# Kernel tuning notes

Hardware: AMD Instinct MI355X
Metric: run time of the kernel (lower is better)

Reference implementation:

```python
import jax, jax.numpy as jnp
import numpy as np

N, L, H, D = 8, 1024, 16, 64
HD = H * D          # hidden_size = 1024
MLP = 4 * HD        # mlp_dim = 4096
EPS = 1e-5


def _layer_norm(x, g, b):
    mu = jnp.mean(x, axis=-1, keepdims=True)
    var = jnp.var(x, axis=-1, keepdims=True)
    return (x - mu) * jax.lax.rsqrt(var + EPS) * g + b


def setup_inputs() -> dict:
    key = jax.random.key(0)
    ks = jax.random.split(key, 8)
    s_in = 1.0 / np.sqrt(HD)
    s_mlp = 1.0 / np.sqrt(MLP)
    return {
        "x": jax.random.normal(ks[0], (N, L, HD), jnp.float32),
        "ln0_g": jnp.ones((HD,), jnp.float32),
        "ln0_b": jnp.zeros((HD,), jnp.float32),
        "wq": jax.random.normal(ks[1], (HD, HD), jnp.float32) * s_in,
        "bq": jnp.zeros((HD,), jnp.float32),
        "wk": jax.random.normal(ks[2], (HD, HD), jnp.float32) * s_in,
        "bk": jnp.zeros((HD,), jnp.float32),
        "wv": jax.random.normal(ks[3], (HD, HD), jnp.float32) * s_in,
        "bv": jnp.zeros((HD,), jnp.float32),
        "wo": jax.random.normal(ks[4], (HD, HD), jnp.float32) * s_in,
        "bo": jnp.zeros((HD,), jnp.float32),
        "ln1_g": jnp.ones((HD,), jnp.float32),
        "ln1_b": jnp.zeros((HD,), jnp.float32),
        "w1": jax.random.normal(ks[5], (HD, MLP), jnp.float32) * s_in,
        "b1": jnp.zeros((MLP,), jnp.float32),
        "w2": jax.random.normal(ks[6], (MLP, HD), jnp.float32) * s_mlp,
        "b2": jnp.zeros((HD,), jnp.float32),
    }


def reference(x, ln0_g, ln0_b, wq, bq, wk, bk, wv, bv, wo, bo,
              ln1_g, ln1_b, w1, b1, w2, b2):
    n, l, hd = x.shape
    # --- pre-LN self-attention ---
    y = _layer_norm(x, ln0_g, ln0_b)
    q = (y @ wq + bq).reshape(n, l, H, D)
    k = (y @ wk + bk).reshape(n, l, H, D)
    v = (y @ wv + bv).reshape(n, l, H, D)
    qkt = jnp.einsum('nqhd,nkhd->nqkh', q, k) / jnp.sqrt(jnp.float32(D))
    attn = jax.nn.softmax(qkt, axis=2)
    y = jnp.einsum('nqkh,nkhd->nqhd', attn, v).reshape(n, l, hd)
    y = y @ wo + bo
    x = x + y  # residual (dropout_rate=0 in eval)
    # --- pre-LN MLP ---
    y = _layer_norm(x, ln1_g, ln1_b)
    y = jax.nn.gelu(y @ w1 + b1)
    y = y @ w2 + b2
    return x + y
```

## Files before the change

kernel.cpp:

```cpp
#include <hip/hip_runtime.h>
#include <math.h>

typedef __attribute__((ext_vector_type(8))) __bf16 bf16x8;
typedef __attribute__((ext_vector_type(4))) float f32x4;

#define NBATCH 8
#define SEQ    1024
#define NHEAD  16
#define DHEAD  64
#define HID    1024
#define MLPD   4096

static __device__ __forceinline__ unsigned short f2bf(float f) {
  unsigned int u = __float_as_uint(f);
  u += 0x7fffu + ((u >> 16) & 1u);
  return (unsigned short)(u >> 16);
}

static __device__ __forceinline__ void gload_lds16(const unsigned short* g,
                                                   unsigned short* l) {
  __builtin_amdgcn_global_load_lds(
      (const __attribute__((address_space(1))) unsigned int*)g,
      (__attribute__((address_space(3))) unsigned int*)l, 16, 0, 0);
}

static __device__ __forceinline__ float gelu_fast(float v) {
  const float z = 0.7978845608028654f * (v + 0.044715f * v * v * v);
  const float e = __expf(-2.0f * fabsf(z));
  float th = (1.0f - e) / (1.0f + e);
  th = copysignf(th, z);
  return 0.5f * v * (1.0f + th);
}

#define MFMA16(a, b, c) __builtin_amdgcn_mfma_f32_16x16x32_bf16(a, b, c, 0, 0, 0)

__global__ __launch_bounds__(256) void k_transpose(const float* __restrict__ in,
                                                   unsigned short* __restrict__ out,
                                                   int R, int C) {
  __shared__ float t[32][33];
  const int tx = threadIdx.x & 31, ty = threadIdx.x >> 5;
  const int c0 = blockIdx.x * 32, r0 = blockIdx.y * 32;
#pragma unroll
  for (int j = 0; j < 4; ++j)
    t[ty + j * 8][tx] = in[(size_t)(r0 + ty + j * 8) * C + c0 + tx];
  __syncthreads();
#pragma unroll
  for (int j = 0; j < 4; ++j)
    out[(size_t)(c0 + ty + j * 8) * R + r0 + tx] = f2bf(t[tx][ty + j * 8]);
}

__global__ void k_pack_bias(const float* __restrict__ bq, const float* __restrict__ bk,
                            const float* __restrict__ bv, float* __restrict__ o) {
  int i = blockIdx.x * 256 + threadIdx.x;
  if (i < 3 * HID) {
    float v = (i < HID) ? bq[i] : (i < 2 * HID ? bk[i - HID] : bv[i - 2 * HID]);
    o[i] = v;
  }
}

__global__ __launch_bounds__(256) void k_ln(const float* __restrict__ x,
                                            const float* __restrict__ gw,
                                            const float* __restrict__ bw,
                                            unsigned short* __restrict__ y) {
  __shared__ float red[2][4];
  const int row = blockIdx.x;
  const int tid = threadIdx.x;
  const float4 v = ((const float4*)(x + (size_t)row * HID))[tid];
  float sum = v.x + v.y + v.z + v.w;
  float sq  = v.x * v.x + v.y * v.y + v.z * v.z + v.w * v.w;
#pragma unroll
  for (int off = 32; off >= 1; off >>= 1) {
    sum += __shfl_xor(sum, off);
    sq  += __shfl_xor(sq, off);
  }
  if ((tid & 63) == 0) { red[0][tid >> 6] = sum; red[1][tid >> 6] = sq; }
  __syncthreads();
  sum = red[0][0] + red[0][1] + red[0][2] + red[0][3];
  sq  = red[1][0] + red[1][1] + red[1][2] + red[1][3];
  const float mu  = sum * (1.0f / HID);
  const float var = sq * (1.0f / HID) - mu * mu;
  const float rs  = rsqrtf(var + 1e-5f);
  const float4 g4 = ((const float4*)gw)[tid];
  const float4 b4 = ((const float4*)bw)[tid];
  ushort4 ov;
  ov.x = f2bf((v.x - mu) * rs * g4.x + b4.x);
  ov.y = f2bf((v.y - mu) * rs * g4.y + b4.y);
  ov.z = f2bf((v.z - mu) * rs * g4.z + b4.z);
  ov.w = f2bf((v.w - mu) * rs * g4.w + b4.w);
  ((ushort4*)(y + (size_t)row * HID))[tid] = ov;
}

template <int EPI, int BN>
__global__ __launch_bounds__(512, 2) void k_gemm(const unsigned short* __restrict__ A,
                                                 const unsigned short* __restrict__ BT,
                                                 const float* __restrict__ bias,
                                                 const float* __restrict__ res,
                                                 void* __restrict__ Cout,
                                                 int M, int N, int K) {
  constexpr int ASZ = 256 * 64;
  constexpr int BSZ = BN * 64;
  constexpr int NF  = BN / 64;
  constexpr int NCW = BN / 4;
  __shared__ unsigned short sh[2 * ASZ + 2 * BSZ];

  const int tid  = threadIdx.x;
  const int lane = tid & 63;
  const int w    = tid >> 6;
  const int wr   = w >> 2, wc = w & 3;
  const int l15  = lane & 15, g = lane >> 4;

  const int gx = gridDim.x;
  const int nwg = gx * gridDim.y;
  int lid = blockIdx.y * gx + blockIdx.x;
  lid = (lid & 7) * (nwg >> 3) + (lid >> 3);
  const int m0 = (lid / gx) * 256, n0 = (lid % gx) * BN;

  f32x4 acc[8][NF] = {};

  const int srow  = w * 8 + (lane >> 3);
  const int scolb = ((lane & 7) * 16) ^ (((lane >> 3) & 7) << 4);
  const unsigned short* pA = A  + (size_t)(m0 + srow) * K + (scolb >> 1);
  const unsigned short* pB = BT + (size_t)(n0 + srow) * K + (scolb >> 1);
  unsigned short* shB = sh + 2 * ASZ;

#define STAGE(buf_, kk)                                                     \
  do {                                                                      \
    _Pragma("unroll") for (int c = 0; c < 4; ++c)                           \
      gload_lds16(pA + (size_t)c * 64 * K + (kk),                           \
                  sh + (buf_) * ASZ + (c * 64 + w * 8) * 64);               \
    _Pragma("unroll") for (int c = 0; c < BN / 64; ++c)                     \
      gload_lds16(pB + (size_t)c * 64 * K + (kk),                           \
                  shB + (buf_) * BSZ + (c * 64 + w * 8) * 64);              \
  } while (0)

  const int fmask = (l15 & 7) << 4;
  const int bo0 = ((0 * 64) + g * 16) ^ fmask;
  const int bo1 = ((1 * 64) + g * 16) ^ fmask;
  const int aRowBase = wr * 128 + l15;
  const int bRowBase = wc * NCW + l15;

  const int NT = K >> 6;

  STAGE(0, 0);
  int buf = 0;
  for (int t = 0; t < NT; ++t) {
    const unsigned short* shAb = sh + buf * ASZ;
    const unsigned short* shBb = shB + buf * BSZ;

    asm volatile("s_waitcnt vmcnt(0)" ::: "memory");
    __builtin_amdgcn_sched_barrier(0);
    __builtin_amdgcn_s_barrier();
    if (t + 1 < NT) STAGE(buf ^ 1, (t + 1) * 64);

    bf16x8 bfr[NF][2];
#pragma unroll
    for (int n = 0; n < NF; ++n) {
      const int br = (bRowBase + n * 16) * 64;
      bfr[n][0] = *(const bf16x8*)(shBb + br + (bo0 >> 1));
      bfr[n][1] = *(const bf16x8*)(shBb + br + (bo1 >> 1));
    }
    bf16x8 afr[8][2];
#pragma unroll
    for (int m = 0; m < 8; ++m) {
      const int ar = (aRowBase + m * 16) * 64;
      afr[m][0] = *(const bf16x8*)(shAb + ar + (bo0 >> 1));
      afr[m][1] = *(const bf16x8*)(shAb + ar + (bo1 >> 1));
    }
    __builtin_amdgcn_sched_barrier(0);

#pragma unroll
    for (int p = 0; p < 4; ++p) {
      __builtin_amdgcn_s_setprio(1);
#pragma unroll
      for (int n = 0; n < NF; ++n) {
        acc[2 * p][n]     = MFMA16(afr[2 * p][0],     bfr[n][0], acc[2 * p][n]);
        acc[2 * p][n]     = MFMA16(afr[2 * p][1],     bfr[n][1], acc[2 * p][n]);
        acc[2 * p + 1][n] = MFMA16(afr[2 * p + 1][0], bfr[n][0], acc[2 * p + 1][n]);
        acc[2 * p + 1][n] = MFMA16(afr[2 * p + 1][1], bfr[n][1], acc[2 * p + 1][n]);
      }
      __builtin_amdgcn_s_setprio(0);
    }
    buf ^= 1;
  }
#undef STAGE

  if constexpr (EPI == 2) {
#pragma unroll
    for (int m = 0; m < 8; ++m) {
#pragma unroll
      for (int n = 0; n < NF; ++n) {
        const int col = n0 + wc * NCW + n * 16 + l15;
        const float bc = bias[col];
#pragma unroll
        for (int r = 0; r < 4; ++r) {
          const int row = m0 + wr * 128 + m * 16 + g * 4 + r;
          const size_t idx = (size_t)row * N + col;
          ((float*)Cout)[idx] = acc[m][n][r] + bc + res[idx];
        }
      }
    }
  } else {
    __builtin_amdgcn_s_barrier();
    unsigned short* ep = sh + w * (128 * NCW);
#pragma unroll
    for (int m = 0; m < 8; ++m) {
#pragma unroll
      for (int n = 0; n < NF; ++n) {
        const float bc = bias[n0 + wc * NCW + n * 16 + l15];
#pragma unroll
        for (int r = 0; r < 4; ++r) {
          float v = acc[m][n][r] + bc;
          if constexpr (EPI == 1) v = gelu_fast(v);
          ep[(m * 16 + g * 4 + r) * NCW + n * 16 + l15] = f2bf(v);
        }
      }
    }
    constexpr int CPR = NCW / 8;
#pragma unroll
    for (int j = 0; j < NCW / 4; ++j) {
      const int t = lane + j * 64;
      const int row = t / CPR, colb = (t % CPR) * 8;
      const uint4 vv = *(const uint4*)(ep + row * NCW + colb);
      unsigned short* outp = (unsigned short*)Cout +
          (size_t)(m0 + wr * 128 + row) * N + n0 + wc * NCW + colb;
      *(uint4*)outp = vv;
    }
  }
}

__global__ __launch_bounds__(256) void k_vt(const unsigned short* __restrict__ qkv,
                                            unsigned short* __restrict__ vT) {
  __shared__ unsigned short t[64][72];
  const int nh = blockIdx.y;
  const int nb = nh >> 4, h = nh & 15;
  const int l0 = blockIdx.x * 64;
  const int tx = threadIdx.x & 7;
  const int ty = threadIdx.x >> 3;
  const unsigned short* src = qkv + (size_t)(nb * SEQ + l0) * 3072 + 2048 + h * DHEAD;
#pragma unroll
  for (int j = 0; j < 2; ++j)
    *(uint4*)(&t[ty + j * 32][tx * 8]) =
        *(const uint4*)(&src[(size_t)(ty + j * 32) * 3072 + tx * 8]);
  __syncthreads();
  unsigned short* dst = vT + (size_t)nh * DHEAD * SEQ + l0;
#pragma unroll
  for (int j = 0; j < 2; ++j) {
    const int d = ty + j * 32;
    ushort4 a, b;
    a.x = t[tx * 8 + 0][d]; a.y = t[tx * 8 + 1][d];
    a.z = t[tx * 8 + 2][d]; a.w = t[tx * 8 + 3][d];
    b.x = t[tx * 8 + 4][d]; b.y = t[tx * 8 + 5][d];
    b.z = t[tx * 8 + 6][d]; b.w = t[tx * 8 + 7][d];
    *(ushort4*)(&dst[(size_t)d * SEQ + tx * 8])     = a;
    *(ushort4*)(&dst[(size_t)d * SEQ + tx * 8 + 4]) = b;
  }
}

#define SOFTMAX_GROUP(S, gq)                                                       \
  {                                                                                \
    float mx = -INFINITY;                                                          \
    _Pragma("unroll") for (int c = 0; c < 4; ++c)                                  \
      _Pragma("unroll") for (int r = 0; r < 4; ++r)                                \
        mx = fmaxf(mx, S[c][r]);                                                   \
    mx = fmaxf(mx, __shfl_xor(mx, 16));                                            \
    mx = fmaxf(mx, __shfl_xor(mx, 32));                                            \
    const float mnew = fmaxf(m_run[gq], mx);                                       \
    const float sc = __expf(0.125f * (m_run[gq] - mnew));                          \
    m_run[gq] = mnew;                                                              \
    float ts = 0.0f;                                                               \
    _Pragma("unroll") for (int c = 0; c < 4; ++c) {                                \
      const float p0 = __expf(0.125f * (S[c][0] - mnew));                          \
      const float p1 = __expf(0.125f * (S[c][1] - mnew));                          \
      const float p2 = __expf(0.125f * (S[c][2] - mnew));                          \
      const float p3 = __expf(0.125f * (S[c][3] - mnew));                          \
      ts += (p0 + p1) + (p2 + p3);                                                 \
      const unsigned int lo = (unsigned int)f2bf(p0) | ((unsigned int)f2bf(p1) << 16); \
      const unsigned int hi = (unsigned int)f2bf(p2) | ((unsigned int)f2bf(p3) << 16); \
      *(uint2*)(&P_lds[w][((gq) * 16 + l15) * 72 + c * 16 + g * 4]) = make_uint2(lo, hi); \
    }                                                                              \
    ts += __shfl_xor(ts, 16);                                                      \
    ts += __shfl_xor(ts, 32);                                                      \
    s_run[gq] = s_run[gq] * sc + ts;                                               \
    const float scr0 = __shfl(sc, g * 4 + 0), scr1 = __shfl(sc, g * 4 + 1);        \
    const float scr2 = __shfl(sc, g * 4 + 2), scr3 = __shfl(sc, g * 4 + 3);        \
    _Pragma("unroll") for (int dt = 0; dt < 4; ++dt) {                             \
      o[gq][dt][0] *= scr0; o[gq][dt][1] *= scr1;                                  \
      o[gq][dt][2] *= scr2; o[gq][dt][3] *= scr3;                                  \
    }                                                                              \
  }

__global__ __launch_bounds__(256, 4) void k_attn(const unsigned short* __restrict__ qkv,
                                                 const unsigned short* __restrict__ vT,
                                                 unsigned short* __restrict__ outp) {
  __shared__ unsigned short Ks[64 * 64];
  __shared__ unsigned short Vs[64 * 64];
  __shared__ unsigned short P_lds[4][32 * 72];
  const int tid  = threadIdx.x;
  const int lane = tid & 63;
  const int w    = tid >> 6;
  const int l15  = lane & 15, g = lane >> 4;
  const int nh = blockIdx.y;
  const int nb = nh >> 4, h = nh & 15;
  const int q0 = blockIdx.x * 128 + w * 32;
  const size_t RS = 3 * HID;

  const unsigned short* Qp = qkv + (size_t)(nb * SEQ + q0) * RS + h * DHEAD;
  const unsigned short* Kg = qkv + (size_t)(nb * SEQ) * RS + HID + h * DHEAD;
  const unsigned short* Vg = vT + (size_t)nh * DHEAD * SEQ;

  const int L0 = tid * 32, L1 = L0 + 16;
  const int kr0 = L0 >> 7, kc0 = (L0 & 127) ^ ((kr0 & 7) << 4);
  const int kr1 = L1 >> 7, kc1 = (L1 & 127) ^ ((kr1 & 7) << 4);

  bf16x8 aq[2][2];
#pragma unroll
  for (int gq = 0; gq < 2; ++gq)
#pragma unroll
    for (int t = 0; t < 2; ++t)
      aq[gq][t] = *(const bf16x8*)(&Qp[(size_t)(gq * 16 + l15) * RS + t * 32 + g * 8]);

  f32x4 o[2][4] = {};
  float m_run[2] = {-INFINITY, -INFINITY};
  float s_run[2] = {0.0f, 0.0f};

  uint4 rk0, rk1, rv0, rv1;
  rk0 = *(const uint4*)(Kg + (size_t)kr0 * RS + (kc0 >> 1));
  rk1 = *(const uint4*)(Kg + (size_t)kr1 * RS + (kc1 >> 1));
  rv0 = *(const uint4*)(Vg + (size_t)kr0 * SEQ + (kc0 >> 1));
  rv1 = *(const uint4*)(Vg + (size_t)kr1 * SEQ + (kc1 >> 1));
  *(uint4*)(&Ks[tid * 16])     = rk0;
  *(uint4*)(&Ks[tid * 16 + 8]) = rk1;
  *(uint4*)(&Vs[tid * 16])     = rv0;
  *(uint4*)(&Vs[tid * 16 + 8]) = rv1;
  __syncthreads();

  const int sw = (l15 & 7) << 4;

  for (int t16 = 0; t16 < 16; ++t16) {
    if (t16 < 15) {
      const int kb = (t16 + 1) * 64;
      rk0 = *(const uint4*)(Kg + (size_t)(kb + kr0) * RS + (kc0 >> 1));
      rk1 = *(const uint4*)(Kg + (size_t)(kb + kr1) * RS + (kc1 >> 1));
      rv0 = *(const uint4*)(Vg + (size_t)kr0 * SEQ + kb + (kc0 >> 1));
      rv1 = *(const uint4*)(Vg + (size_t)kr1 * SEQ + kb + (kc1 >> 1));
    }

    f32x4 S0[4], S1[4];
#pragma unroll
    for (int c = 0; c < 4; ++c) {
      const int krow = c * 16 + l15;
      const bf16x8 k0 = *(const bf16x8*)(&Ks[krow * 64 + ((( 0 + g * 16) ^ sw) >> 1)]);
      const bf16x8 k1 = *(const bf16x8*)(&Ks[krow * 64 + (((64 + g * 16) ^ sw) >> 1)]);
      f32x4 a = {};
      a = MFMA16(k0, aq[0][0], a);
      a = MFMA16(k1, aq[0][1], a);
      S0[c] = a;
      f32x4 b = {};
      b = MFMA16(k0, aq[1][0], b);
      b = MFMA16(k1, aq[1][1], b);
      S1[c] = b;
    }

    SOFTMAX_GROUP(S0, 0)
    SOFTMAX_GROUP(S1, 1)

    bf16x8 pa[2][2];
#pragma unroll
    for (int gq = 0; gq < 2; ++gq)
#pragma unroll
      for (int th = 0; th < 2; ++th)
        pa[gq][th] = *(const bf16x8*)(&P_lds[w][(gq * 16 + l15) * 72 + th * 32 + g * 8]);
#pragma unroll
    for (int dt = 0; dt < 4; ++dt) {
      const int vrow = dt * 16 + l15;
      const bf16x8 v0 = *(const bf16x8*)(&Vs[vrow * 64 + ((( 0 + g * 16) ^ sw) >> 1)]);
      const bf16x8 v1 = *(const bf16x8*)(&Vs[vrow * 64 + (((64 + g * 16) ^ sw) >> 1)]);
      o[0][dt] = MFMA16(pa[0][0], v0, o[0][dt]);
      o[0][dt] = MFMA16(pa[0][1], v1, o[0][dt]);
      o[1][dt] = MFMA16(pa[1][0], v0, o[1][dt]);
      o[1][dt] = MFMA16(pa[1][1], v1, o[1][dt]);
    }
    __syncthreads();
    if (t16 < 15) {
      *(uint4*)(&Ks[tid * 16])     = rk0;
      *(uint4*)(&Ks[tid * 16 + 8]) = rk1;
      *(uint4*)(&Vs[tid * 16])     = rv0;
      *(uint4*)(&Vs[tid * 16 + 8]) = rv1;
      __syncthreads();
    }
  }

#pragma unroll
  for (int gq = 0; gq < 2; ++gq) {
    float sr[4];
#pragma unroll
    for (int r = 0; r < 4; ++r) sr[r] = 1.0f / __shfl(s_run[gq], g * 4 + r);
#pragma unroll
    for (int dt = 0; dt < 4; ++dt)
#pragma unroll
      for (int r = 0; r < 4; ++r)
        outp[(size_t)(nb * SEQ + q0 + gq * 16 + g * 4 + r) * HID + h * DHEAD + dt * 16 + l15] =
            f2bf(o[gq][dt][r] * sr[r]);
  }
}

extern "C" void kernel_launch(void* const* d_in, const int* in_sizes, int n_in,
                              void* d_out, int out_size, void* d_ws, size_t ws_size,
                              hipStream_t stream) {
  const float* x    = (const float*)d_in[0];
  const float* ln0g = (const float*)d_in[1];
  const float* ln0b = (const float*)d_in[2];
  const float* wq   = (const float*)d_in[3];
  const float* bq   = (const float*)d_in[4];
  const float* wk   = (const float*)d_in[5];
  const float* bk   = (const float*)d_in[6];
  const float* wv   = (const float*)d_in[7];
  const float* bv   = (const float*)d_in[8];
  const float* wo   = (const float*)d_in[9];
  const float* bo   = (const float*)d_in[10];
  const float* ln1g = (const float*)d_in[11];
  const float* ln1b = (const float*)d_in[12];
  const float* w1   = (const float*)d_in[13];
  const float* b1   = (const float*)d_in[14];
  const float* w2   = (const float*)d_in[15];
  const float* b2   = (const float*)d_in[16];
  float* out = (float*)d_out;

  char* ws = (char*)d_ws;
  unsigned short* qkvT = (unsigned short*)(ws + 0);
  unsigned short* woT  = (unsigned short*)(ws + 6291456);
  unsigned short* w1T  = (unsigned short*)(ws + 8388608);
  unsigned short* w2T  = (unsigned short*)(ws + 16777216);
  float*          bqkv = (float*)(ws + 25165824);
  unsigned short* ybuf = (unsigned short*)(ws + 25178112);
  unsigned short* qkv  = (unsigned short*)(ws + 41955328);
  unsigned short* att  = (unsigned short*)(ws + 92286976);
  unsigned short* hbuf = qkv;
  unsigned short* vT   = ybuf;

  const int M = NBATCH * SEQ;

  k_transpose<<<dim3(32, 32),  256, 0, stream>>>(wq, qkvT,                        HID,  HID);
  k_transpose<<<dim3(32, 32),  256, 0, stream>>>(wk, qkvT + (size_t)1024 * HID,   HID,  HID);
  k_transpose<<<dim3(32, 32),  256, 0, stream>>>(wv, qkvT + (size_t)2048 * HID,   HID,  HID);
  k_transpose<<<dim3(32, 32),  256, 0, stream>>>(wo, woT,                         HID,  HID);
  k_transpose<<<dim3(128, 32), 256, 0, stream>>>(w1, w1T,                         HID,  MLPD);
  k_transpose<<<dim3(32, 128), 256, 0, stream>>>(w2, w2T,                         MLPD, HID);
  k_pack_bias<<<dim3(12), 256, 0, stream>>>(bq, bk, bv, bqkv);

  k_ln<<<dim3(M), 256, 0, stream>>>(x, ln0g, ln0b, ybuf);
  k_gemm<0, 128><<<dim3(24, 32), 512, 0, stream>>>(ybuf, qkvT, bqkv, nullptr, (void*)qkv, M, 3 * HID, HID);
  k_vt<<<dim3(16, 128), 256, 0, stream>>>(qkv, vT);
  k_attn<<<dim3(8, 128), 256, 0, stream>>>(qkv, vT, att);
  k_gemm<2, 128><<<dim3(8, 32), 512, 0, stream>>>(att, woT, bo, x, (void*)out, M, HID, HID);
  k_ln<<<dim3(M), 256, 0, stream>>>(out, ln1g, ln1b, ybuf);
  k_gemm<1, 256><<<dim3(16, 32), 512, 0, stream>>>(ybuf, w1T, b1, nullptr, (void*)hbuf, M, MLPD, HID);
  k_gemm<2, 128><<<dim3(8, 32), 512, 0, stream>>>(hbuf, w2T, b2, out, (void*)out, M, HID, MLPD);
}
```

Before: 376.8 us.

## Triple-buffer GEMM LDS staging and fix BN at 128 for all GEMMs

Moves the GEMM mainloop from double to triple buffering. Tiles are prefetched two steps ahead, and a partial vmcnt wait lets one stage's loads stay in flight while the current tile is computed. BN is fixed at 128, so the MLP-up GEMM now uses 128-wide tiles with twice as many workgroups. LDS use per block grows to 3*(32KB+16KB)=144KB, which likely allows only one block per CU instead of two. Occupancy and latency hiding across waves may drop as a result.

```diff
diff --git a/kernel.cpp b/kernel.cpp
--- a/kernel.cpp
+++ b/kernel.cpp
@@ -90,18 +90,20 @@
   ((ushort4*)(y + (size_t)row * HID))[tid] = ov;
 }
 
-template <int EPI, int BN>
+template <int EPI>
 __global__ __launch_bounds__(512, 2) void k_gemm(const unsigned short* __restrict__ A,
                                                  const unsigned short* __restrict__ BT,
                                                  const float* __restrict__ bias,
                                                  const float* __restrict__ res,
                                                  void* __restrict__ Cout,
                                                  int M, int N, int K) {
+  constexpr int BN  = 128;
   constexpr int ASZ = 256 * 64;
   constexpr int BSZ = BN * 64;
-  constexpr int NF  = BN / 64;
-  constexpr int NCW = BN / 4;
-  __shared__ unsigned short sh[2 * ASZ + 2 * BSZ];
+  constexpr int NF  = 2;
+  constexpr int NCW = 32;
+  __shared__ unsigned short As[3][ASZ];
+  __shared__ unsigned short Bs[3][BSZ];
 
   const int tid  = threadIdx.x;
   const int lane = tid & 63;
@@ -121,16 +123,14 @@
   const int scolb = ((lane & 7) * 16) ^ (((lane >> 3) & 7) << 4);
   const unsigned short* pA = A  + (size_t)(m0 + srow) * K + (scolb >> 1);
   const unsigned short* pB = BT + (size_t)(n0 + srow) * K + (scolb >> 1);
-  unsigned short* shB = sh + 2 * ASZ;
-
-#define STAGE(buf_, kk)                                                     \
+
+#define STAGE(b_, kk)                                                       \
   do {                                                                      \
+    gload_lds16(pB + (kk),                     &Bs[b_][(0 * 64 + w * 8) * 64]); \
+    gload_lds16(pB + (size_t)64 * K + (kk),    &Bs[b_][(1 * 64 + w * 8) * 64]); \
     _Pragma("unroll") for (int c = 0; c < 4; ++c)                           \
       gload_lds16(pA + (size_t)c * 64 * K + (kk),                           \
-                  sh + (buf_) * ASZ + (c * 64 + w * 8) * 64);               \
-    _Pragma("unroll") for (int c = 0; c < BN / 64; ++c)                     \
-      gload_lds16(pB + (size_t)c * 64 * K + (kk),                           \
-                  shB + (buf_) * BSZ + (c * 64 + w * 8) * 64);              \
+                  &As[b_][(c * 64 + w * 8) * 64]);                          \
   } while (0)
 
   const int fmask = (l15 & 7) << 4;
@@ -142,15 +142,20 @@
   const int NT = K >> 6;
 
   STAGE(0, 0);
-  int buf = 0;
+  STAGE(1, 64);
+
+  int bcur = 0;
   for (int t = 0; t < NT; ++t) {
-    const unsigned short* shAb = sh + buf * ASZ;
-    const unsigned short* shBb = shB + buf * BSZ;
-
-    asm volatile("s_waitcnt vmcnt(0)" ::: "memory");
+    if (t + 1 < NT) { asm volatile("s_waitcnt vmcnt(6)" ::: "memory"); }
+    else            { asm volatile("s_waitcnt vmcnt(0)" ::: "memory"); }
     __builtin_amdgcn_sched_barrier(0);
     __builtin_amdgcn_s_barrier();
-    if (t + 1 < NT) STAGE(buf ^ 1, (t + 1) * 64);
+
+    const int bn2 = (bcur + 2 >= 3) ? bcur - 1 : bcur + 2;
+    if (t + 2 < NT) STAGE(bn2, (t + 2) * 64);
+
+    const unsigned short* shAb = &As[bcur][0];
+    const unsigned short* shBb = &Bs[bcur][0];
 
     bf16x8 bfr[NF][2];
 #pragma unroll
@@ -180,7 +185,7 @@
       }
       __builtin_amdgcn_s_setprio(0);
     }
-    buf ^= 1;
+    bcur = (bcur + 1 >= 3) ? 0 : bcur + 1;
   }
 #undef STAGE
 
@@ -201,7 +206,7 @@
     }
   } else {
     __builtin_amdgcn_s_barrier();
-    unsigned short* ep = sh + w * (128 * NCW);
+    unsigned short* ep = &As[0][0] + w * (128 * NCW);
 #pragma unroll
     for (int m = 0; m < 8; ++m) {
 #pragma unroll
@@ -449,11 +454,11 @@
   k_pack_bias<<<dim3(12), 256, 0, stream>>>(bq, bk, bv, bqkv);
 
   k_ln<<<dim3(M), 256, 0, stream>>>(x, ln0g, ln0b, ybuf);
-  k_gemm<0, 128><<<dim3(24, 32), 512, 0, stream>>>(ybuf, qkvT, bqkv, nullptr, (void*)qkv, M, 3 * HID, HID);
+  k_gemm<0><<<dim3(24, 32), 512, 0, stream>>>(ybuf, qkvT, bqkv, nullptr, (void*)qkv, M, 3 * HID, HID);
   k_vt<<<dim3(16, 128), 256, 0, stream>>>(qkv, vT);
   k_attn<<<dim3(8, 128), 256, 0, stream>>>(qkv, vT, att);
-  k_gemm<2, 128><<<dim3(8, 32), 512, 0, stream>>>(att, woT, bo, x, (void*)out, M, HID, HID);
+  k_gemm<2><<<dim3(8, 32), 512, 0, stream>>>(att, woT, bo, x, (void*)out, M, HID, HID);
   k_ln<<<dim3(M), 256, 0, stream>>>(out, ln1g, ln1b, ybuf);
-  k_gemm<1, 256><<<dim3(16, 32), 512, 0, stream>>>(ybuf, w1T, b1, nullptr, (void*)hbuf, M, MLPD, HID);
-  k_gemm<2, 128><<<dim3(8, 32), 512, 0, stream>>>(hbuf, w2T, b2, out, (void*)out, M, HID, MLPD);
-}
+  k_gemm<1><<<dim3(32, 32), 512, 0, stream>>>(ybuf, w1T, b1, nullptr, (void*)hbuf, M, MLPD, HID);
+  k_gemm<2><<<dim3(8, 32), 512, 0, stream>>>(hbuf, w2T, b2, out, (void*)out, M, HID, MLPD);
+}
```

New measurement: 433.4 us. +15.0%, slower.

## Add 256x256 GEMM kernel with interleaved LDS loads and MFMA phases

Applied to the files above, without the earlier changes.

Adds a dedicated 256x256-tile GEMM kernel that splits each K-step into four MFMA phases. Next-tile global-to-LDS loads for B and A are issued between phases, with explicit waitcnt, barriers and setprio around the MFMA bursts. The QKV projection now uses 256-wide tiles instead of 128, and the FC1 GEMM moves to the new kernel. The aim is better overlap of memory and compute and more data reuse per tile. The cost is more barriers and higher register pressure. The epilogue stages bf16 output through LDS so global stores are coalesced.

```diff
diff --git a/kernel.cpp b/kernel.cpp
--- a/kernel.cpp
+++ b/kernel.cpp
@@ -90,17 +90,191 @@
   ((ushort4*)(y + (size_t)row * HID))[tid] = ov;
 }
 
-template <int EPI, int BN>
+template <int EPI>
+__global__ __launch_bounds__(512, 2) void k_gemm256(const unsigned short* __restrict__ A,
+                                                    const unsigned short* __restrict__ BT,
+                                                    const float* __restrict__ bias,
+                                                    void* __restrict__ Cout,
+                                                    int M, int N, int K) {
+  constexpr int ASZ = 256 * 64;
+  constexpr int BSZ = 256 * 64;
+  __shared__ unsigned short sh[2 * ASZ + 2 * BSZ];
+
+  const int tid  = threadIdx.x;
+  const int lane = tid & 63;
+  const int w    = tid >> 6;
+  const int wr   = w >> 2, wc = w & 3;
+  const int l15  = lane & 15, g = lane >> 4;
+
+  const int gx = gridDim.x;
+  const int nwg = gx * gridDim.y;
+  int lid = blockIdx.y * gx + blockIdx.x;
+  lid = (lid & 7) * (nwg >> 3) + (lid >> 3);
+  const int m0 = (lid / gx) * 256, n0 = (lid % gx) * 256;
+
+  f32x4 acc[8][4] = {};
+
+  const int srow  = tid >> 3;
+  const int scolb = ((tid & 7) * 16) ^ ((srow & 7) << 4);
+  const unsigned short* pA = A  + (size_t)(m0 + srow) * K + (scolb >> 1);
+  const unsigned short* pB = BT + (size_t)(n0 + srow) * K + (scolb >> 1);
+  unsigned short* shA = sh;
+  unsigned short* shB = sh + 2 * ASZ;
+
+#define SAH(h, b_, kk)                                                            \
+  gload_lds16(pA + (size_t)((h) * 128) * K + (kk),                                \
+              &shA[(b_) * ASZ + ((h) * 128 + w * 8) * 64]);                       \
+  gload_lds16(pA + (size_t)((h) * 128 + 64) * K + (kk),                           \
+              &shA[(b_) * ASZ + ((h) * 128 + 64 + w * 8) * 64]);
+#define SBH(h, b_, kk)                                                            \
+  gload_lds16(pB + (size_t)((h) * 128) * K + (kk),                                \
+              &shB[(b_) * BSZ + ((h) * 128 + w * 8) * 64]);                       \
+  gload_lds16(pB + (size_t)((h) * 128 + 64) * K + (kk),                           \
+              &shB[(b_) * BSZ + ((h) * 128 + 64 + w * 8) * 64]);
+
+  const int fmask = (l15 & 7) << 4;
+  const int bo0 = (g * 16) ^ fmask;
+  const int bo1 = (64 + g * 16) ^ fmask;
+  const int aRow = wr * 128 + l15;
+  const int bRow = wc * 64 + l15;
+
+  const int NT = K >> 6;
+
+  SAH(0, 0, 0) SAH(1, 0, 0) SBH(0, 0, 0) SBH(1, 0, 0)
+  SAH(0, 1, 64) SAH(1, 1, 64) SBH(0, 1, 64) SBH(1, 1, 64)
+
+  for (int t = 0; t < NT; ++t) {
+    const int buf = t & 1;
+    const unsigned short* Ab = shA + buf * ASZ;
+    const unsigned short* Bb = shB + buf * BSZ;
+    const int nxt = (t + 2) * 64;
+    const bool more = (t + 2 < NT);
+
+    if (t + 1 < NT) { asm volatile("s_waitcnt vmcnt(8)" ::: "memory"); }
+    else            { asm volatile("s_waitcnt vmcnt(0)" ::: "memory"); }
+    __builtin_amdgcn_sched_barrier(0);
+    __builtin_amdgcn_s_barrier();
+
+    bf16x8 alo[4][2], ahi[4][2], bf[4][2];
+
+#pragma unroll
+    for (int m = 0; m < 4; ++m) {
+      const int ar = (aRow + m * 16) * 64;
+      alo[m][0] = *(const bf16x8*)(Ab + ar + (bo0 >> 1));
+      alo[m][1] = *(const bf16x8*)(Ab + ar + (bo1 >> 1));
+    }
+#pragma unroll
+    for (int n = 0; n < 2; ++n) {
+      const int br = (bRow + n * 16) * 64;
+      bf[n][0] = *(const bf16x8*)(Bb + br + (bo0 >> 1));
+      bf[n][1] = *(const bf16x8*)(Bb + br + (bo1 >> 1));
+    }
+    __builtin_amdgcn_s_barrier();
+    asm volatile("s_waitcnt lgkmcnt(0)" ::: "memory");
+    __builtin_amdgcn_sched_barrier(0);
+    __builtin_amdgcn_s_setprio(1);
+#pragma unroll
+    for (int m = 0; m < 4; ++m)
+#pragma unroll
+      for (int n = 0; n < 2; ++n) {
+        acc[m][n] = MFMA16(alo[m][0], bf[n][0], acc[m][n]);
+        acc[m][n] = MFMA16(alo[m][1], bf[n][1], acc[m][n]);
+      }
+    __builtin_amdgcn_s_setprio(0);
+    __builtin_amdgcn_s_barrier();
+
+#pragma unroll
+    for (int n = 2; n < 4; ++n) {
+      const int br = (bRow + n * 16) * 64;
+      bf[n][0] = *(const bf16x8*)(Bb + br + (bo0 >> 1));
+      bf[n][1] = *(const bf16x8*)(Bb + br + (bo1 >> 1));
+    }
+    __builtin_amdgcn_s_barrier();
+    asm volatile("s_waitcnt lgkmcnt(0)" ::: "memory");
+    __builtin_amdgcn_sched_barrier(0);
+    __builtin_amdgcn_s_setprio(1);
+#pragma unroll
+    for (int m = 0; m < 4; ++m)
+#pragma unroll
+      for (int n = 2; n < 4; ++n) {
+        acc[m][n] = MFMA16(alo[m][0], bf[n][0], acc[m][n]);
+        acc[m][n] = MFMA16(alo[m][1], bf[n][1], acc[m][n]);
+      }
+    __builtin_amdgcn_s_setprio(0);
+    __builtin_amdgcn_s_barrier();
+
+#pragma unroll
+    for (int m = 0; m < 4; ++m) {
+      const int ar = (aRow + (4 + m) * 16) * 64;
+      ahi[m][0] = *(const bf16x8*)(Ab + ar + (bo0 >> 1));
+      ahi[m][1] = *(const bf16x8*)(Ab + ar + (bo1 >> 1));
+    }
+    if (more) { SBH(0, buf, nxt) SBH(1, buf, nxt) }
+    __builtin_amdgcn_s_barrier();
+    asm volatile("s_waitcnt lgkmcnt(0)" ::: "memory");
+    __builtin_amdgcn_sched_barrier(0);
+    __builtin_amdgcn_s_setprio(1);
+#pragma unroll
+    for (int m = 0; m < 4; ++m)
+#pragma unroll
+      for (int n = 2; n < 4; ++n) {
+        acc[4 + m][n] = MFMA16(ahi[m][0], bf[n][0], acc[4 + m][n]);
+        acc[4 + m][n] = MFMA16(ahi[m][1], bf[n][1], acc[4 + m][n]);
+      }
+    __builtin_amdgcn_s_setprio(0);
+    __builtin_amdgcn_s_barrier();
+
+    if (more) { SAH(0, buf, nxt) SAH(1, buf, nxt) }
+    __builtin_amdgcn_s_setprio(1);
+#pragma unroll
+    for (int m = 0; m < 4; ++m)
+#pragma unroll
+      for (int n = 0; n < 2; ++n) {
+        acc[4 + m][n] = MFMA16(ahi[m][0], bf[n][0], acc[4 + m][n]);
+        acc[4 + m][n] = MFMA16(ahi[m][1], bf[n][1], acc[4 + m][n]);
+      }
+    __builtin_amdgcn_s_setprio(0);
+    __builtin_amdgcn_s_barrier();
+  }
+#undef SAH
+#undef SBH
+
+  unsigned short* ep = sh + w * (128 * 64);
+#pragma unroll
+  for (int m = 0; m < 8; ++m)
+#pragma unroll
+    for (int n = 0; n < 4; ++n) {
+      const float bc = bias[n0 + wc * 64 + n * 16 + l15];
+#pragma unroll
+      for (int r = 0; r < 4; ++r) {
+        float v = acc[m][n][r] + bc;
+        if constexpr (EPI == 1) v = gelu_fast(v);
+        ep[(m * 16 + g * 4 + r) * 64 + n * 16 + l15] = f2bf(v);
+      }
+    }
+#pragma unroll
+  for (int j = 0; j < 16; ++j) {
+    const int t2 = lane + j * 64;
+    const int row = t2 >> 3, colb = (t2 & 7) * 8;
+    const uint4 vv = *(const uint4*)(ep + row * 64 + colb);
+    unsigned short* outp = (unsigned short*)Cout +
+        (size_t)(m0 + wr * 128 + row) * N + n0 + wc * 64 + colb;
+    *(uint4*)outp = vv;
+  }
+}
+
+template <int EPI>
 __global__ __launch_bounds__(512, 2) void k_gemm(const unsigned short* __restrict__ A,
                                                  const unsigned short* __restrict__ BT,
                                                  const float* __restrict__ bias,
                                                  const float* __restrict__ res,
                                                  void* __restrict__ Cout,
                                                  int M, int N, int K) {
+  constexpr int BN  = 128;
   constexpr int ASZ = 256 * 64;
   constexpr int BSZ = BN * 64;
-  constexpr int NF  = BN / 64;
-  constexpr int NCW = BN / 4;
+  constexpr int NF  = 2;
+  constexpr int NCW = 32;
   __shared__ unsigned short sh[2 * ASZ + 2 * BSZ];
 
   const int tid  = threadIdx.x;
@@ -449,11 +623,11 @@
   k_pack_bias<<<dim3(12), 256, 0, stream>>>(bq, bk, bv, bqkv);
 
   k_ln<<<dim3(M), 256, 0, stream>>>(x, ln0g, ln0b, ybuf);
-  k_gemm<0, 128><<<dim3(24, 32), 512, 0, stream>>>(ybuf, qkvT, bqkv, nullptr, (void*)qkv, M, 3 * HID, HID);
+  k_gemm256<0><<<dim3(12, 32), 512, 0, stream>>>(ybuf, qkvT, bqkv, (void*)qkv, M, 3 * HID, HID);
   k_vt<<<dim3(16, 128), 256, 0, stream>>>(qkv, vT);
   k_attn<<<dim3(8, 128), 256, 0, stream>>>(qkv, vT, att);
-  k_gemm<2, 128><<<dim3(8, 32), 512, 0, stream>>>(att, woT, bo, x, (void*)out, M, HID, HID);
+  k_gemm<2><<<dim3(8, 32), 512, 0, stream>>>(att, woT, bo, x, (void*)out, M, HID, HID);
   k_ln<<<dim3(M), 256, 0, stream>>>(out, ln1g, ln1b, ybuf);
-  k_gemm<1, 256><<<dim3(16, 32), 512, 0, stream>>>(ybuf, w1T, b1, nullptr, (void*)hbuf, M, MLPD, HID);
-  k_gemm<2, 128><<<dim3(8, 32), 512, 0, stream>>>(hbuf, w2T, b2, out, (void*)out, M, HID, MLPD);
-}
+  k_gemm256<1><<<dim3(16, 32), 512, 0, stream>>>(ybuf, w1T, b1, (void*)hbuf, M, MLPD, HID);
+  k_gemm<2><<<dim3(8, 32), 512, 0, stream>>>(hbuf, w2T, b2, out, (void*)out, M, HID, MLPD);
+}
```

Result: no change. 382.0 us (+1.4%).
